# Optimization experiments

Hardware: AMD Instinct MI355X
Metric: run time of the kernel (lower is better)

## Reference

```python
import jax, jax.numpy as jnp
import numpy as np

LN_EPS = 1e-5  # torch LayerNorm default


def setup_inputs() -> dict:
    key = jax.random.key(0)
    ks = jax.random.split(key, 6)
    N, E, D = 50000, 800000, 128
    x = jax.random.normal(ks[0], (N, D), dtype=jnp.float32)
    edge_index = jax.random.randint(ks[1], (2, E), 0, N, dtype=jnp.int64)
    # Linear params (torch default-ish init scale)
    W = jax.random.normal(ks[2], (D, D), dtype=jnp.float32) / np.sqrt(D)
    b = jax.random.normal(ks[3], (D,), dtype=jnp.float32) * 0.01
    # LayerNorm params
    gamma = jnp.ones((D,), dtype=jnp.float32)
    beta = jnp.zeros((D,), dtype=jnp.float32)
    return {"x": x, "edge_index": edge_index, "W": W, "b": b,
            "gamma": gamma, "beta": beta}


def reference(x, edge_index, W, b, gamma, beta):
    N = x.shape[0]
    # add_self_loops
    loops = jnp.arange(N, dtype=edge_index.dtype)
    row = jnp.concatenate([edge_index[0], loops])  # sources (x_j)
    col = jnp.concatenate([edge_index[1], loops])  # targets (aggregate here)

    h = x @ W.T + b  # [N, D]

    # symmetric normalization: deg computed on row, includes self loops (deg>=1)
    deg = jax.ops.segment_sum(jnp.ones(row.shape, dtype=h.dtype), row,
                              num_segments=N)
    dis = deg ** -0.5
    norm = dis[row] * dis[col]  # [E+N]

    # gather-scale-scatter message passing (aggr='add')
    msg = norm[:, None] * h[row]              # [E+N, D]
    agg = jax.ops.segment_sum(msg, col, num_segments=N)  # [N, D]

    out = jax.nn.relu(agg)
    # dropout: identity (eval mode)
    mu = jnp.mean(out, axis=-1, keepdims=True)
    var = jnp.var(out, axis=-1, keepdims=True)
    out = (out - mu) * jax.lax.rsqrt(var + LN_EPS) * gamma + beta
    return out + x  # residual (in_channels == out_channels, no proj)
```

## Files before the change

### kernel.cpp

```cpp
#include <hip/hip_runtime.h>


#define D 128
#define CHSH 15
#define CHUNK (1 << CHSH)
#define NWORD 12500

typedef short bf16x8 __attribute__((ext_vector_type(8)));
typedef float f32x4 __attribute__((ext_vector_type(4)));

__device__ __forceinline__ unsigned short f2bf(float f) {
    unsigned u = __float_as_uint(f);
    return (unsigned short)((u + 0x7fffu + ((u >> 16) & 1u)) >> 16);
}
__device__ __forceinline__ float bf2f_lo(unsigned v) { return __uint_as_float(v << 16); }
__device__ __forceinline__ float bf2f_hi(unsigned v) { return __uint_as_float(v & 0xffff0000u); }

__global__ void __launch_bounds__(1024)
k_gemm_hist(const float* __restrict__ x, const float* __restrict__ W,
            const float* __restrict__ bias, unsigned short* __restrict__ hb,
            int nrows,
            const int* __restrict__ ei, int E, int n,
            unsigned char* __restrict__ degc, unsigned char* __restrict__ cntc,
            unsigned char* __restrict__ aux, int K) {
    __shared__ unsigned sm[NWORD];
    int bid = blockIdx.x;
    if (bid < 2 * K) {
        unsigned* hist = sm;
        bool is_cnt = bid < K;
        int c = is_cnt ? bid : bid - K;
        const int* vs = is_cnt ? (ei + E) : ei;
        for (int i = threadIdx.x; i < NWORD; i += 1024) hist[i] = 0u;
        __syncthreads();
        int e0 = c << CHSH;
        int e1 = e0 + CHUNK; if (e1 > E) e1 = E;
        if (is_cnt) {
            for (int e = e0 + threadIdx.x; e < e1; e += 1024) {
                int v = vs[e];
                unsigned sh = (v & 3) * 8;
                unsigned old = atomicAdd(&hist[v >> 2], 1u << sh);
                aux[e] = (unsigned char)(old >> sh);
            }
        } else {
            for (int e = e0 + threadIdx.x; e < e1; e += 1024) {
                int v = vs[e];
                atomicAdd(&hist[v >> 2], 1u << ((v & 3) * 8));
            }
        }
        __syncthreads();
        unsigned* dst = (unsigned*)((is_cnt ? cntc : degc) + (size_t)c * n);
        for (int i = threadIdx.x; i < NWORD; i += 1024) dst[i] = hist[i];
    } else {
        unsigned short* wf = (unsigned short*)sm;
        for (int s = threadIdx.x; s < D * D; s += 1024) {
            int j  = s & 7;
            int ln = (s >> 3) & 63;
            int g  = s >> 9;
            int kt = g & 3, nt = g >> 2;
            int rw = nt * 16 + (ln & 15);
            int cl = kt * 32 + (ln >> 4) * 8 + j;
            wf[s] = f2bf(W[rw * D + cl]);
        }
        __syncthreads();

        int wid = threadIdx.x >> 6, lane = threadIdx.x & 63;
        int m0 = (bid - 2 * K) * 256 + wid * 16;
        if (m0 >= nrows) return;
        int lo16 = lane & 15, quad = lane >> 4;
        const float* arow = x + (size_t)(m0 + lo16) * D + quad * 8;
        bf16x8 a[4];
        #pragma unroll
        for (int kt = 0; kt < 4; kt++) {
            float4 p = *(const float4*)(arow + kt * 32);
            float4 q = *(const float4*)(arow + kt * 32 + 4);
            bf16x8 av;
            av[0] = (short)f2bf(p.x); av[1] = (short)f2bf(p.y);
            av[2] = (short)f2bf(p.z); av[3] = (short)f2bf(p.w);
            av[4] = (short)f2bf(q.x); av[5] = (short)f2bf(q.y);
            av[6] = (short)f2bf(q.z); av[7] = (short)f2bf(q.w);
            a[kt] = av;
        }
        const bf16x8* wfv = (const bf16x8*)wf;
        #pragma unroll
        for (int nt = 0; nt < 8; nt++) {
            int n0 = nt * 16;
            float bj = bias[n0 + lo16];
            f32x4 acc = {bj, bj, bj, bj};
            #pragma unroll
            for (int kt = 0; kt < 4; kt++) {
                bf16x8 b = wfv[(nt * 4 + kt) * 64 + lane];
                acc = __builtin_amdgcn_mfma_f32_16x16x32_bf16(a[kt], b, acc, 0, 0, 0);
            }
            #pragma unroll
            for (int r = 0; r < 4; r++) {
                int gr = m0 + quad * 4 + r;
                hb[(size_t)gr * D + n0 + lo16] = f2bf(acc[r]);
            }
        }
    }
}

__global__ void k_partial(const unsigned char* __restrict__ degc,
                          const unsigned char* __restrict__ cntc,
                          float* __restrict__ dis, unsigned* __restrict__ cnt,
                          unsigned* __restrict__ partial, int n, int K) {
    __shared__ unsigned s[256];
    int t = threadIdx.x;
    int i = blockIdx.x * 256 + t;
    unsigned tot = 0;
    if (i < n) {
        unsigned d = 0;
        for (int c = 0; c < K; c++)
            d += __builtin_nontemporal_load(degc + (size_t)c * n + i);
        dis[i] = rsqrtf((float)d + 1.0f);
        for (int c = 0; c < K; c++) tot += cntc[(size_t)c * n + i];
        cnt[i] = tot;
    }
    s[t] = tot;
    __syncthreads();
    #pragma unroll
    for (int d = 128; d > 0; d >>= 1) {
        if (t < d) s[t] += s[t + d];
        __syncthreads();
    }
    if (t == 0) partial[blockIdx.x] = s[0];
}

__global__ void k_rowptrc(const unsigned* __restrict__ cnt, const unsigned char* __restrict__ cntc,
                          const unsigned* __restrict__ partial, int n, int E,
                          int* __restrict__ rowptr, int* __restrict__ rowptrc, int K, int nb) {
    __shared__ unsigned ps[256];
    __shared__ unsigned base_sh;
    int t = threadIdx.x;
    unsigned pv = (t < nb) ? partial[t] : 0u;
    ps[t] = pv;
    __syncthreads();
    #pragma unroll
    for (int d = 1; d < 256; d <<= 1) {
        unsigned u = (t >= d) ? ps[t - d] : 0u;
        __syncthreads();
        ps[t] += u;
        __syncthreads();
    }
    if (t == blockIdx.x) base_sh = ps[t] - pv;
    __syncthreads();
    unsigned bbase = base_sh;
    int i = blockIdx.x * 256 + t;
    unsigned v = (i < n) ? cnt[i] : 0u;
    ps[t] = v;
    __syncthreads();
    #pragma unroll
    for (int d = 1; d < 256; d <<= 1) {
        unsigned u = (t >= d) ? ps[t - d] : 0u;
        __syncthreads();
        ps[t] += u;
        __syncthreads();
    }
    if (i < n) {
        int base = (int)(bbase + ps[t] - v);
        rowptr[i] = base;
        unsigned run = 0;
        for (int c = 0; c < K; c++) {
            rowptrc[(size_t)c * n + i] = base + (int)run;
            run += cntc[(size_t)c * n + i];
        }
    }
    if (blockIdx.x == 0 && t == 0) rowptr[n] = E;
}

__global__ void k_fill(const int* __restrict__ ei, int E, int n,
                       const int* __restrict__ rowptrc, const unsigned char* __restrict__ aux,
                       int* __restrict__ srcs) {
    int e = blockIdx.x * 256 + threadIdx.x;
    if (e < E) {
        int r = __builtin_nontemporal_load(ei + e);
        int v = __builtin_nontemporal_load(ei + E + e);
        int c = e >> CHSH;
        int rank = __builtin_nontemporal_load(aux + e);
        srcs[rowptrc[(size_t)c * n + v] + rank] = r;
    }
}

__global__ void k_agg(const float* __restrict__ x, const unsigned short* __restrict__ hb,
                      const float* __restrict__ dis,
                      const int* __restrict__ rowptr, const int* __restrict__ srcs,
                      const float* __restrict__ gamma, const float* __restrict__ beta,
                      float* __restrict__ out, int n) {
    int wid = threadIdx.x >> 6, lane = threadIdx.x & 63;
    int row = blockIdx.x * 4 + wid;
    if (row >= n) return;
    int q = lane >> 4, t = lane & 15;
    float dc = dis[row];
    float acc[8];
    #pragma unroll
    for (int i = 0; i < 8; i++) acc[i] = 0.0f;
    if (q == 0) {
        uint4 u = ((const uint4*)(hb + (size_t)row * D))[t];
        float sn = dc * dc;
        acc[0] = sn * bf2f_lo(u.x); acc[1] = sn * bf2f_hi(u.x);
        acc[2] = sn * bf2f_lo(u.y); acc[3] = sn * bf2f_hi(u.y);
        acc[4] = sn * bf2f_lo(u.z); acc[5] = sn * bf2f_hi(u.z);
        acc[6] = sn * bf2f_lo(u.w); acc[7] = sn * bf2f_hi(u.w);
    }
    int s0 = rowptr[row];
    int len = rowptr[row + 1] - s0;
    for (int base = 0; base < len; base += 64) {
        int idx = base + lane;
        int sv = (idx < len) ? __builtin_nontemporal_load(srcs + s0 + idx) : 0;
        float dv = (idx < len) ? dis[sv] : 0.0f;
        int m = len - base; if (m > 64) m = 64;
        int kmax = (m + 3) >> 2;
        int gcount = (kmax + 3) >> 2;
        for (int gg = 0; gg < gcount; gg++) {
            int jb = q + (gg << 4);
            int r0 = __shfl(sv, jb, 64);
            int r1 = __shfl(sv, jb + 4, 64);
            int r2 = __shfl(sv, jb + 8, 64);
            int r3 = __shfl(sv, jb + 12, 64);
            float w0 = dc * __shfl(dv, jb, 64);
            float w1 = dc * __shfl(dv, jb + 4, 64);
            float w2 = dc * __shfl(dv, jb + 8, 64);
            float w3 = dc * __shfl(dv, jb + 12, 64);
            uint4 u0 = ((const uint4*)(hb + ((size_t)r0 << 7)))[t];
            uint4 u1 = ((const uint4*)(hb + ((size_t)r1 << 7)))[t];
            uint4 u2 = ((const uint4*)(hb + ((size_t)r2 << 7)))[t];
            uint4 u3 = ((const uint4*)(hb + ((size_t)r3 << 7)))[t];
            acc[0] += w0 * bf2f_lo(u0.x); acc[1] += w0 * bf2f_hi(u0.x);
            acc[2] += w0 * bf2f_lo(u0.y); acc[3] += w0 * bf2f_hi(u0.y);
            acc[4] += w0 * bf2f_lo(u0.z); acc[5] += w0 * bf2f_hi(u0.z);
            acc[6] += w0 * bf2f_lo(u0.w); acc[7] += w0 * bf2f_hi(u0.w);
            acc[0] += w1 * bf2f_lo(u1.x); acc[1] += w1 * bf2f_hi(u1.x);
            acc[2] += w1 * bf2f_lo(u1.y); acc[3] += w1 * bf2f_hi(u1.y);
            acc[4] += w1 * bf2f_lo(u1.z); acc[5] += w1 * bf2f_hi(u1.z);
            acc[6] += w1 * bf2f_lo(u1.w); acc[7] += w1 * bf2f_hi(u1.w);
            acc[0] += w2 * bf2f_lo(u2.x); acc[1] += w2 * bf2f_hi(u2.x);
            acc[2] += w2 * bf2f_lo(u2.y); acc[3] += w2 * bf2f_hi(u2.y);
            acc[4] += w2 * bf2f_lo(u2.z); acc[5] += w2 * bf2f_hi(u2.z);
            acc[6] += w2 * bf2f_lo(u2.w); acc[7] += w2 * bf2f_hi(u2.w);
            acc[0] += w3 * bf2f_lo(u3.x); acc[1] += w3 * bf2f_hi(u3.x);
            acc[2] += w3 * bf2f_lo(u3.y); acc[3] += w3 * bf2f_hi(u3.y);
            acc[4] += w3 * bf2f_lo(u3.z); acc[5] += w3 * bf2f_hi(u3.z);
            acc[6] += w3 * bf2f_lo(u3.w); acc[7] += w3 * bf2f_hi(u3.w);
        }
    }
    #pragma unroll
    for (int i = 0; i < 8; i++) {
        acc[i] += __shfl_xor(acc[i], 16, 64);
        acc[i] += __shfl_xor(acc[i], 32, 64);
        acc[i] = acc[i] > 0.0f ? acc[i] : 0.0f;
    }
    float s1r = 0.0f, s2r = 0.0f;
    #pragma unroll
    for (int i = 0; i < 8; i++) { s1r += acc[i]; s2r += acc[i] * acc[i]; }
    #pragma unroll
    for (int mm = 8; mm >= 1; mm >>= 1) {
        s1r += __shfl_xor(s1r, mm, 64);
        s2r += __shfl_xor(s2r, mm, 64);
    }
    float mean = s1r * (1.0f / 128.0f);
    float var  = s2r * (1.0f / 128.0f) - mean * mean;
    float rstd = rsqrtf(var + 1e-5f);
    if (q == 0) {
        const f32x4* gr = (const f32x4*)gamma;
        const f32x4* br = (const f32x4*)beta;
        const f32x4* xr = (const f32x4*)(x + (size_t)row * D);
        f32x4* orow = (f32x4*)(out + (size_t)row * D);
        #pragma unroll
        for (int hf = 0; hf < 2; hf++) {
            f32x4 g = gr[2 * t + hf], b = br[2 * t + hf];
            f32x4 xx = __builtin_nontemporal_load(xr + 2 * t + hf);
            f32x4 o;
            o[0] = (acc[4 * hf + 0] - mean) * rstd * g[0] + b[0] + xx[0];
            o[1] = (acc[4 * hf + 1] - mean) * rstd * g[1] + b[1] + xx[1];
            o[2] = (acc[4 * hf + 2] - mean) * rstd * g[2] + b[2] + xx[2];
            o[3] = (acc[4 * hf + 3] - mean) * rstd * g[3] + b[3] + xx[3];
            __builtin_nontemporal_store(o, orow + 2 * t + hf);
        }
    }
}

extern "C" void kernel_launch(void* const* d_in, const int* in_sizes, int n_in,
                              void* d_out, int out_size, void* d_ws, size_t ws_size,
                              hipStream_t stream) {
    const float* x     = (const float*)d_in[0];
    const int*   ei    = (const int*)d_in[1];
    const float* W     = (const float*)d_in[2];
    const float* bias  = (const float*)d_in[3];
    const float* gamma = (const float*)d_in[4];
    const float* beta  = (const float*)d_in[5];
    int N = in_sizes[0] / D;
    int E = in_sizes[1] / 2;
    int nb  = (N + 255) / 256;
    int nbE = (E + 255) / 256;
    int K   = (E + CHUNK - 1) >> CHSH;
    int gemm_blocks = (N + 255) / 256;

    char* ws = (char*)d_ws;
    size_t off = 0;
    unsigned short* hb  = (unsigned short*)(ws + off); off += (size_t)N * D * 2;
    unsigned char* degc = (unsigned char*)(ws + off);  off += (size_t)K * N;
    unsigned char* cntc = (unsigned char*)(ws + off);  off += (size_t)K * N;
    float*    dis       = (float*)(ws + off);          off += (size_t)N * 4;
    unsigned* cnt       = (unsigned*)(ws + off);       off += (size_t)N * 4;
    int*      rowptr    = (int*)(ws + off);            off += (size_t)(N + 1) * 4;
    int*      rowptrc   = (int*)(ws + off);            off += (size_t)K * N * 4;
    unsigned* partial   = (unsigned*)(ws + off);       off += 256 * 4;
    unsigned char* aux  = (unsigned char*)(ws + off);  off += (size_t)E;
    int*      srcs      = (int*)(ws + off);            off += (size_t)E * 4;
    float*    out       = (float*)d_out;

    k_gemm_hist<<<2 * K + gemm_blocks, 1024, 0, stream>>>(x, W, bias, hb, N,
                                                          ei, E, N, degc, cntc, aux, K);
    k_partial<<<nb, 256, 0, stream>>>(degc, cntc, dis, cnt, partial, N, K);
    k_rowptrc<<<nb, 256, 0, stream>>>(cnt, cntc, partial, N, E, rowptr, rowptrc, K, nb);
    k_fill<<<nbE, 256, 0, stream>>>(ei, E, N, rowptrc, aux, srcs);
    k_agg<<<(N + 3) / 4, 256, 0, stream>>>(x, hb, dis, rowptr, srcs, gamma, beta, out, N);
}
```

Baseline: 177.6 us.

## Split each aggregation row across two wavefronts by feature halves

```diff
diff --git a/kernel.cpp b/kernel.cpp
--- a/kernel.cpp
+++ b/kernel.cpp
@@ -80,7 +80,7 @@
             av[6] = (short)f2bf(q.z); av[7] = (short)f2bf(q.w);
             a[kt] = av;
         }
-        const bf16x8* wfv = (const bf16x8*)wf;
+        const bf16x8* wfv = (const bf16x8*)sm;
         #pragma unroll
         for (int nt = 0; nt < 8; nt++) {
             int n0 = nt * 16;
@@ -186,24 +186,27 @@
                       const int* __restrict__ rowptr, const int* __restrict__ srcs,
                       const float* __restrict__ gamma, const float* __restrict__ beta,
                       float* __restrict__ out, int n) {
+    __shared__ float sh[8];
     int wid = threadIdx.x >> 6, lane = threadIdx.x & 63;
-    int row = blockIdx.x * 4 + wid;
-    if (row >= n) return;
+    int row = blockIdx.x * 2 + (wid >> 1);
+    int half = wid & 1;
+    bool valid = row < n;
     int q = lane >> 4, t = lane & 15;
-    float dc = dis[row];
-    float acc[8];
-    #pragma unroll
-    for (int i = 0; i < 8; i++) acc[i] = 0.0f;
-    if (q == 0) {
-        uint4 u = ((const uint4*)(hb + (size_t)row * D))[t];
+    const uint2* hbh = (const uint2*)hb;
+    unsigned hbase = ((unsigned)(valid ? row : 0) << 5) + (half << 4) + t;
+    float acc[4];
+    #pragma unroll
+    for (int i = 0; i < 4; i++) acc[i] = 0.0f;
+    float dc = valid ? dis[row] : 0.0f;
+    if (q == 0 && valid) {
+        uint2 u = hbh[hbase];
         float sn = dc * dc;
         acc[0] = sn * bf2f_lo(u.x); acc[1] = sn * bf2f_hi(u.x);
         acc[2] = sn * bf2f_lo(u.y); acc[3] = sn * bf2f_hi(u.y);
-        acc[4] = sn * bf2f_lo(u.z); acc[5] = sn * bf2f_hi(u.z);
-        acc[6] = sn * bf2f_lo(u.w); acc[7] = sn * bf2f_hi(u.w);
-    }
-    int s0 = rowptr[row];
-    int len = rowptr[row + 1] - s0;
+    }
+    int s0 = 0, len = 0;
+    if (valid) { s0 = rowptr[row]; len = rowptr[row + 1] - s0; }
+    unsigned hoff = (half << 4) + t;
     for (int base = 0; base < len; base += 64) {
         int idx = base + lane;
         int sv = (idx < len) ? __builtin_nontemporal_load(srcs + s0 + idx) : 0;
@@ -221,61 +224,55 @@
             float w1 = dc * __shfl(dv, jb + 4, 64);
             float w2 = dc * __shfl(dv, jb + 8, 64);
             float w3 = dc * __shfl(dv, jb + 12, 64);
-            uint4 u0 = ((const uint4*)(hb + ((size_t)r0 << 7)))[t];
-            uint4 u1 = ((const uint4*)(hb + ((size_t)r1 << 7)))[t];
-            uint4 u2 = ((const uint4*)(hb + ((size_t)r2 << 7)))[t];
-            uint4 u3 = ((const uint4*)(hb + ((size_t)r3 << 7)))[t];
+            uint2 u0 = hbh[((unsigned)r0 << 5) + hoff];
+            uint2 u1 = hbh[((unsigned)r1 << 5) + hoff];
+            uint2 u2 = hbh[((unsigned)r2 << 5) + hoff];
+            uint2 u3 = hbh[((unsigned)r3 << 5) + hoff];
             acc[0] += w0 * bf2f_lo(u0.x); acc[1] += w0 * bf2f_hi(u0.x);
             acc[2] += w0 * bf2f_lo(u0.y); acc[3] += w0 * bf2f_hi(u0.y);
-            acc[4] += w0 * bf2f_lo(u0.z); acc[5] += w0 * bf2f_hi(u0.z);
-            acc[6] += w0 * bf2f_lo(u0.w); acc[7] += w0 * bf2f_hi(u0.w);
             acc[0] += w1 * bf2f_lo(u1.x); acc[1] += w1 * bf2f_hi(u1.x);
             acc[2] += w1 * bf2f_lo(u1.y); acc[3] += w1 * bf2f_hi(u1.y);
-            acc[4] += w1 * bf2f_lo(u1.z); acc[5] += w1 * bf2f_hi(u1.z);
-            acc[6] += w1 * bf2f_lo(u1.w); acc[7] += w1 * bf2f_hi(u1.w);
             acc[0] += w2 * bf2f_lo(u2.x); acc[1] += w2 * bf2f_hi(u2.x);
             acc[2] += w2 * bf2f_lo(u2.y); acc[3] += w2 * bf2f_hi(u2.y);
-            acc[4] += w2 * bf2f_lo(u2.z); acc[5] += w2 * bf2f_hi(u2.z);
-            acc[6] += w2 * bf2f_lo(u2.w); acc[7] += w2 * bf2f_hi(u2.w);
             acc[0] += w3 * bf2f_lo(u3.x); acc[1] += w3 * bf2f_hi(u3.x);
             acc[2] += w3 * bf2f_lo(u3.y); acc[3] += w3 * bf2f_hi(u3.y);
-            acc[4] += w3 * bf2f_lo(u3.z); acc[5] += w3 * bf2f_hi(u3.z);
-            acc[6] += w3 * bf2f_lo(u3.w); acc[7] += w3 * bf2f_hi(u3.w);
-        }
-    }
-    #pragma unroll
-    for (int i = 0; i < 8; i++) {
+        }
+    }
+    #pragma unroll
+    for (int i = 0; i < 4; i++) {
         acc[i] += __shfl_xor(acc[i], 16, 64);
         acc[i] += __shfl_xor(acc[i], 32, 64);
         acc[i] = acc[i] > 0.0f ? acc[i] : 0.0f;
     }
-    float s1r = 0.0f, s2r = 0.0f;
-    #pragma unroll
-    for (int i = 0; i < 8; i++) { s1r += acc[i]; s2r += acc[i] * acc[i]; }
+    float s1 = 0.0f, s2 = 0.0f;
+    #pragma unroll
+    for (int i = 0; i < 4; i++) { s1 += acc[i]; s2 += acc[i] * acc[i]; }
     #pragma unroll
     for (int mm = 8; mm >= 1; mm >>= 1) {
-        s1r += __shfl_xor(s1r, mm, 64);
-        s2r += __shfl_xor(s2r, mm, 64);
-    }
-    float mean = s1r * (1.0f / 128.0f);
-    float var  = s2r * (1.0f / 128.0f) - mean * mean;
+        s1 += __shfl_xor(s1, mm, 64);
+        s2 += __shfl_xor(s2, mm, 64);
+    }
+    if (lane == 0) { sh[wid * 2] = s1; sh[wid * 2 + 1] = s2; }
+    __syncthreads();
+    s1 += sh[(wid ^ 1) * 2];
+    s2 += sh[(wid ^ 1) * 2 + 1];
+    float mean = s1 * (1.0f / 128.0f);
+    float var  = s2 * (1.0f / 128.0f) - mean * mean;
     float rstd = rsqrtf(var + 1e-5f);
-    if (q == 0) {
+    if (q == 0 && valid) {
+        unsigned ci = (half << 4) + t;
         const f32x4* gr = (const f32x4*)gamma;
         const f32x4* br = (const f32x4*)beta;
         const f32x4* xr = (const f32x4*)(x + (size_t)row * D);
         f32x4* orow = (f32x4*)(out + (size_t)row * D);
-        #pragma unroll
-        for (int hf = 0; hf < 2; hf++) {
-            f32x4 g = gr[2 * t + hf], b = br[2 * t + hf];
-            f32x4 xx = __builtin_nontemporal_load(xr + 2 * t + hf);
-            f32x4 o;
-            o[0] = (acc[4 * hf + 0] - mean) * rstd * g[0] + b[0] + xx[0];
-            o[1] = (acc[4 * hf + 1] - mean) * rstd * g[1] + b[1] + xx[1];
-            o[2] = (acc[4 * hf + 2] - mean) * rstd * g[2] + b[2] + xx[2];
-            o[3] = (acc[4 * hf + 3] - mean) * rstd * g[3] + b[3] + xx[3];
-            __builtin_nontemporal_store(o, orow + 2 * t + hf);
-        }
+        f32x4 g = gr[ci], b = br[ci];
+        f32x4 xx = __builtin_nontemporal_load(xr + ci);
+        f32x4 o;
+        o[0] = (acc[0] - mean) * rstd * g[0] + b[0] + xx[0];
+        o[1] = (acc[1] - mean) * rstd * g[1] + b[1] + xx[1];
+        o[2] = (acc[2] - mean) * rstd * g[2] + b[2] + xx[2];
+        o[3] = (acc[3] - mean) * rstd * g[3] + b[3] + xx[3];
+        __builtin_nontemporal_store(o, orow + ci);
     }
 }
 
@@ -314,5 +311,5 @@
     k_partial<<<nb, 256, 0, stream>>>(degc, cntc, dis, cnt, partial, N, K);
     k_rowptrc<<<nb, 256, 0, stream>>>(cnt, cntc, partial, N, E, rowptr, rowptrc, K, nb);
     k_fill<<<nbE, 256, 0, stream>>>(ei, E, N, rowptrc, aux, srcs);
-    k_agg<<<(N + 3) / 4, 256, 0, stream>>>(x, hb, dis, rowptr, srcs, gamma, beta, out, N);
-}
+    k_agg<<<(N + 1) / 2, 256, 0, stream>>>(x, hb, dis, rowptr, srcs, gamma, beta, out, N);
+}
```

Measured after the change: 198.0 us. 11.4% more time.
